# Kernel optimization log

Hardware: AMD Instinct MI355X
Metric: run time of the kernel (lower is better)

The kernel has to match this reference:

```python
import jax, jax.numpy as jnp
import numpy as np

NUM_SAMPLES = 128  # from __init__ default


def _trilinear_sample(vox, g):
    """grid_sample 5D, mode=bilinear (trilinear), padding_mode=zeros, align_corners=True.
    vox: [C, Dv, Hv, Wv]; g: [P, 3] normalized (x,y,z) with x->Wv, y->Hv, z->Dv.
    Returns [P, C]."""
    C, D, Hh, Ww = vox.shape
    x = (g[:, 0] + 1.0) * 0.5 * (Ww - 1)
    y = (g[:, 1] + 1.0) * 0.5 * (Hh - 1)
    z = (g[:, 2] + 1.0) * 0.5 * (D - 1)
    x0 = jnp.floor(x); y0 = jnp.floor(y); z0 = jnp.floor(z)
    xd = x - x0; yd = y - y0; zd = z - z0
    x0i = x0.astype(jnp.int32); y0i = y0.astype(jnp.int32); z0i = z0.astype(jnp.int32)
    out = jnp.zeros((g.shape[0], C), vox.dtype)
    for dz, wz in ((0, 1.0 - zd), (1, zd)):
        for dy, wy in ((0, 1.0 - yd), (1, yd)):
            for dx, wx in ((0, 1.0 - xd), (1, xd)):
                zi = z0i + dz; yi = y0i + dy; xi = x0i + dx
                valid = ((zi >= 0) & (zi < D) & (yi >= 0) & (yi < Hh) & (xi >= 0) & (xi < Ww)).astype(vox.dtype)
                zc = jnp.clip(zi, 0, D - 1); yc = jnp.clip(yi, 0, Hh - 1); xc = jnp.clip(xi, 0, Ww - 1)
                vals = vox[:, zc, yc, xc]  # [C, P]
                out = out + ((wz * wy * wx * valid)[:, None]) * vals.T
    return out


def setup_inputs() -> dict:
    key = jax.random.key(0)
    k1, k2 = jax.random.split(key)
    B, Hv, Wv, Dv = 4, 128, 128, 128
    H, W = 128, 128
    rgbsigma = jax.random.uniform(k1, (B, Hv, Wv, Dv, 4), dtype=jnp.float32)
    # cameras at ~z=3 looking down -z (identity rotation), slightly jittered
    pose = jnp.tile(jnp.eye(4, dtype=jnp.float32), (B, 1, 1))
    trans = jnp.array([0.0, 0.0, 3.0], dtype=jnp.float32) + 0.1 * jax.random.normal(k2, (B, 3), dtype=jnp.float32)
    pose = pose.at[:, :3, 3].set(trans)
    K = jnp.tile(jnp.array([[150.0, 0.0, 64.0], [0.0, 150.0, 64.0], [0.0, 0.0, 1.0]], dtype=jnp.float32), (B, 1, 1))
    bbox_min = jnp.tile(jnp.array([-1.0, -1.0, -1.0], dtype=jnp.float32), (B, 1))
    bbox_max = jnp.tile(jnp.array([1.0, 1.0, 1.0], dtype=jnp.float32), (B, 1))
    return {"rgbsigma": rgbsigma, "camera_pose": pose, "camera_intrinsics": K,
            "bbox_min": bbox_min, "bbox_max": bbox_max, "H": H, "W": W}


def reference(rgbsigma, camera_pose, camera_intrinsics, bbox_min, bbox_max, H, W):
    B = camera_pose.shape[0]
    N = H * W
    # --- ray generation ---
    ii, jj = jnp.meshgrid(jnp.arange(H, dtype=jnp.float32), jnp.arange(W, dtype=jnp.float32), indexing='ij')
    ii = ii.reshape(-1); jj = jj.reshape(-1)  # [N]
    fx = camera_intrinsics[:, 0, 0][:, None]; fy = camera_intrinsics[:, 1, 1][:, None]
    cx = camera_intrinsics[:, 0, 2][:, None]; cy = camera_intrinsics[:, 1, 2][:, None]
    dirs = jnp.stack([(jj[None, :] - cx) / fx, -(ii[None, :] - cy) / fy,
                      -jnp.ones((B, N), dtype=jnp.float32)], axis=-1)  # [B,N,3]
    rays_d = jnp.einsum('bij,bnj->bni', camera_pose[:, :3, :3], dirs)
    rays_d = rays_d / jnp.maximum(jnp.linalg.norm(rays_d, axis=-1, keepdims=True), 1e-12)
    rays_o = jnp.broadcast_to(camera_pose[:, None, :3, 3], (B, N, 3))
    # --- near/far via slab test ---
    inv_d = 1.0 / (rays_d + 1e-10)
    bmin = bbox_min[:, None, :]; bmax = bbox_max[:, None, :]
    t_min = (bmin - rays_o) * inv_d; t_max = (bmax - rays_o) * inv_d
    t1 = jnp.minimum(t_min, t_max); t2 = jnp.maximum(t_min, t_max)
    near = jnp.maximum(jnp.max(t1, axis=-1, keepdims=True), 0.1)
    far = jnp.maximum(jnp.min(t2, axis=-1, keepdims=True), near + 0.1)
    # --- stratified-uniform sample points ---
    t_vals = jnp.linspace(0.0, 1.0, NUM_SAMPLES, dtype=jnp.float32)
    z_vals = near + (far - near) * t_vals  # [B,N,M]
    pts = rays_o[:, :, None, :] + rays_d[:, :, None, :] * z_vals[..., None]  # [B,N,M,3]
    # --- trilinear voxel query ---
    scale = (bbox_max - bbox_min + 1e-10)[:, None, None, :]
    pts_norm = 2.0 * (pts - bbox_min[:, None, None, :]) / scale - 1.0
    vox = jnp.transpose(rgbsigma, (0, 4, 3, 1, 2))  # [B,4,Dv,Hv,Wv]
    sampled = jax.vmap(_trilinear_sample)(vox, pts_norm.reshape(B, N * NUM_SAMPLES, 3))
    sampled = sampled.reshape(B, N, NUM_SAMPLES, 4)
    rgb = sampled[..., :3]; sigma = sampled[..., 3]
    # --- alpha compositing ---
    dists = z_vals[..., 1:] - z_vals[..., :-1]
    dists = jnp.concatenate([dists, jnp.full_like(dists[..., :1], 1e10)], axis=-1)
    alpha = 1.0 - jnp.exp(-jax.nn.relu(sigma) * dists)
    trans = jnp.cumprod(jnp.concatenate([jnp.ones_like(alpha[..., :1]), 1.0 - alpha + 1e-10], axis=-1), axis=-1)[..., :-1]
    weights = alpha * trans
    rgb_map = jnp.sum(weights[..., None] * rgb, axis=-2)  # [B,N,3]
    acc_map = jnp.sum(weights, axis=-1)
    rgb_map = rgb_map + (1.0 - acc_map[..., None])  # white background
    return jnp.transpose(rgb_map.reshape(B, H, W, 3), (0, 3, 1, 2))
```

## Files before the change

### kernel.cpp

```cpp
#include <hip/hip_runtime.h>

#define NSAMP 128
#define VD 128

struct Corner8 {
    float4 v0, v1, v2, v3, v4, v5, v6, v7;
    float  w0, w1, w2, w3, w4, w5, w6, w7;
};

__device__ __forceinline__ void compute_ray_setup(
    int ray, int N, int W,
    const float* __restrict__ pose, const float* __restrict__ Kmat,
    const float* __restrict__ bmin, const float* __restrict__ bmax,
    float& axv, float& bxv, float& ayv, float& byv, float& azv, float& bzv,
    float& near, float& dt)
{
    const int b = ray / N;
    const int pix = ray - b * N;
    const int i = pix / W;
    const int j = pix - i * W;

    const float* P  = pose + b * 16;
    const float* Kb = Kmat + b * 9;
    const float fx = Kb[0], cx = Kb[2], fy = Kb[4], cy = Kb[5];

    const float dcx = ((float)j - cx) / fx;
    const float dcy = -((float)i - cy) / fy;
    const float dcz = -1.0f;

    float dx = P[0]*dcx + P[1]*dcy + P[2]*dcz;
    float dy = P[4]*dcx + P[5]*dcy + P[6]*dcz;
    float dz = P[8]*dcx + P[9]*dcy + P[10]*dcz;
    float nrm = sqrtf(dx*dx + dy*dy + dz*dz);
    nrm = fmaxf(nrm, 1e-12f);
    dx /= nrm; dy /= nrm; dz /= nrm;

    const float ox = P[3], oy = P[7], oz = P[11];

    const float bx0 = bmin[b*3+0], by0 = bmin[b*3+1], bz0 = bmin[b*3+2];
    const float bx1 = bmax[b*3+0], by1 = bmax[b*3+1], bz1 = bmax[b*3+2];

    const float ivx = 1.0f / (dx + 1e-10f);
    const float ivy = 1.0f / (dy + 1e-10f);
    const float ivz = 1.0f / (dz + 1e-10f);

    float ta, tb;
    ta = (bx0 - ox) * ivx; tb = (bx1 - ox) * ivx;
    const float t1x = fminf(ta, tb), t2x = fmaxf(ta, tb);
    ta = (by0 - oy) * ivy; tb = (by1 - oy) * ivy;
    const float t1y = fminf(ta, tb), t2y = fmaxf(ta, tb);
    ta = (bz0 - oz) * ivz; tb = (bz1 - oz) * ivz;
    const float t1z = fminf(ta, tb), t2z = fmaxf(ta, tb);

    near = fmaxf(fmaxf(t1x, fmaxf(t1y, t1z)), 0.1f);
    const float far = fmaxf(fminf(t2x, fminf(t2y, t2z)), near + 0.1f);

    const float sxs = (bx1 - bx0) + 1e-10f;
    const float sys = (by1 - by0) + 1e-10f;
    const float szs = (bz1 - bz0) + 1e-10f;
    const float C = (float)(VD - 1);
    axv = (ox - bx0) / sxs * C; bxv = dx / sxs * C;
    ayv = (oy - by0) / sys * C; byv = dy / sys * C;
    azv = (oz - bz0) / szs * C; bzv = dz / szs * C;

    dt = (far - near) * (1.0f / (float)(NSAMP - 1));
}

__global__ __launch_bounds__(256)
void RaySetup_kernel(const float* __restrict__ pose,
                     const float* __restrict__ Kmat,
                     const float* __restrict__ bmin,
                     const float* __restrict__ bmax,
                     const int* __restrict__ dH,
                     const int* __restrict__ dW,
                     float* __restrict__ rp,
                     int rays)
{
    const int ray = blockIdx.x * blockDim.x + threadIdx.x;
    if (ray >= rays) return;
    const int H = dH[0], W = dW[0];
    const int N = H * W;
    float axv, bxv, ayv, byv, azv, bzv, near, dt;
    compute_ray_setup(ray, N, W, pose, Kmat, bmin, bmax,
                      axv, bxv, ayv, byv, azv, bzv, near, dt);
    float4* o = reinterpret_cast<float4*>(rp + (size_t)ray * 8);
    o[0] = make_float4(axv, bxv, ayv, byv);
    o[1] = make_float4(azv, bzv, near, dt);
}

__device__ __forceinline__ void fetch_sample(
    Corner8& Bf, const float4* __restrict__ V4, float t,
    float axv, float bxv, float ayv, float byv, float azv, float bzv)
{
    const float xf = axv + bxv * t;
    const float yf = ayv + byv * t;
    const float zf = azv + bzv * t;
    const float x0f = floorf(xf), y0f = floorf(yf), z0f = floorf(zf);
    const float xd = xf - x0f, yd = yf - y0f, zd = zf - z0f;
    const int x0 = (int)x0f, y0 = (int)y0f, z0 = (int)z0f;
    const int x1 = x0 + 1, y1 = y0 + 1, z1 = z0 + 1;

    const int xc0 = min(max(x0, 0), VD - 1), xc1 = min(max(x1, 0), VD - 1);
    const int yc0 = min(max(y0, 0), VD - 1), yc1 = min(max(y1, 0), VD - 1);
    const int zc0 = min(max(z0, 0), VD - 1), zc1 = min(max(z1, 0), VD - 1);

    const float vx0 = (x0 == xc0) ? 1.0f : 0.0f;
    const float vx1 = (x1 == xc1) ? 1.0f : 0.0f;
    const float vy0 = (y0 == yc0) ? 1.0f : 0.0f;
    const float vy1 = (y1 == yc1) ? 1.0f : 0.0f;
    const float vz0 = (z0 == zc0) ? 1.0f : 0.0f;
    const float vz1 = (z1 == zc1) ? 1.0f : 0.0f;

    const float wx0 = (1.0f - xd) * vx0, wx1 = xd * vx1;
    const float wy0 = (1.0f - yd) * vy0, wy1 = yd * vy1;
    const float wz0 = (1.0f - zd) * vz0, wz1 = zd * vz1;

    const int r0 = yc0 << 14, r1 = yc1 << 14;
    const int c0 = xc0 << 7,  c1 = xc1 << 7;
    const int i00 = r0 + c0, i01 = r0 + c1;
    const int i10 = r1 + c0, i11 = r1 + c1;

    Bf.v0 = V4[i00 + zc0];
    Bf.v1 = V4[i00 + zc1];
    Bf.v2 = V4[i01 + zc0];
    Bf.v3 = V4[i01 + zc1];
    Bf.v4 = V4[i10 + zc0];
    Bf.v5 = V4[i10 + zc1];
    Bf.v6 = V4[i11 + zc0];
    Bf.v7 = V4[i11 + zc1];

    Bf.w0 = wy0 * wx0 * wz0;
    Bf.w1 = wy0 * wx0 * wz1;
    Bf.w2 = wy0 * wx1 * wz0;
    Bf.w3 = wy0 * wx1 * wz1;
    Bf.w4 = wy1 * wx0 * wz0;
    Bf.w5 = wy1 * wx0 * wz1;
    Bf.w6 = wy1 * wx1 * wz0;
    Bf.w7 = wy1 * wx1 * wz1;
}

__device__ __forceinline__ float4 interp_sample(const Corner8& Bf)
{
    float4 r;
    r.x = (Bf.w0*Bf.v0.x + Bf.w1*Bf.v1.x) + (Bf.w2*Bf.v2.x + Bf.w3*Bf.v3.x)
        + (Bf.w4*Bf.v4.x + Bf.w5*Bf.v5.x) + (Bf.w6*Bf.v6.x + Bf.w7*Bf.v7.x);
    r.y = (Bf.w0*Bf.v0.y + Bf.w1*Bf.v1.y) + (Bf.w2*Bf.v2.y + Bf.w3*Bf.v3.y)
        + (Bf.w4*Bf.v4.y + Bf.w5*Bf.v5.y) + (Bf.w6*Bf.v6.y + Bf.w7*Bf.v7.y);
    r.z = (Bf.w0*Bf.v0.z + Bf.w1*Bf.v1.z) + (Bf.w2*Bf.v2.z + Bf.w3*Bf.v3.z)
        + (Bf.w4*Bf.v4.z + Bf.w5*Bf.v5.z) + (Bf.w6*Bf.v6.z + Bf.w7*Bf.v7.z);
    r.w = (Bf.w0*Bf.v0.w + Bf.w1*Bf.v1.w) + (Bf.w2*Bf.v2.w + Bf.w3*Bf.v3.w)
        + (Bf.w4*Bf.v4.w + Bf.w5*Bf.v5.w) + (Bf.w6*Bf.v6.w + Bf.w7*Bf.v7.w);
    return r;
}

__device__ __forceinline__ void consume_set(
    const Corner8& C, int k, float dt, int sl,
    float& Tcarry, float& accR, float& accG, float& accB)
{
    const float4 s = interp_sample(C);
    const float sig = fmaxf(s.w, 0.0f);
    const float dist = (k == NSAMP - 1) ? 1e10f : dt;
    const float alpha = 1.0f - __expf(-sig * dist);
    float incl = 1.0f - alpha + 1e-10f;

    #pragma unroll
    for (int d = 1; d < 16; d <<= 1) {
        const float o = __shfl_up(incl, d, 16);
        if (sl >= d) incl *= o;
    }
    float P = __shfl_up(incl, 1, 16);
    if (sl == 0) P = 1.0f;

    const float w = alpha * P * Tcarry;
    accR += w * s.x;
    accG += w * s.y;
    accB += w * s.z;

    const float Ttot = __shfl(incl, 15, 16);
    Tcarry *= Ttot;
}

template <bool USE_WS>
__global__ __launch_bounds__(256, 1)
void VoxelRenderer_kernel(const float* __restrict__ vol,
                          const float* __restrict__ pose,
                          const float* __restrict__ Kmat,
                          const float* __restrict__ bmin,
                          const float* __restrict__ bmax,
                          const int* __restrict__ dH,
                          const int* __restrict__ dW,
                          const float* __restrict__ rayp,
                          float* __restrict__ out,
                          int rays)
{
    const int lane = threadIdx.x & 63;
    const int wq   = threadIdx.x >> 6;
    const int rq   = lane >> 4;
    const int sl   = lane & 15;

    const int nwg = gridDim.x;
    const int bid = blockIdx.x;
    const int q = nwg >> 3, r = nwg & 7;
    const int xcd = bid & 7, idx = bid >> 3;
    const int swz = (xcd < r ? xcd * (q + 1) : r * (q + 1) + (xcd - r) * q) + idx;

    const int H = dH[0], W = dW[0];
    const int N = H * W;
    const int quads = rays >> 2;
    const int qid = swz * 4 + wq;
    if (qid >= quads) return;

    const int qPerImg = N >> 2;
    const int b   = qid / qPerImg;
    const int rem = qid - b * qPerImg;
    const int halfW = W >> 1;
    const int qi = rem / halfW;
    const int qj = rem - qi * halfW;
    const int i = qi * 2 + (rq >> 1);
    const int j = qj * 2 + (rq & 1);
    const int ray = b * N + i * W + j;

    float axv, bxv, ayv, byv, azv, bzv, near, dt;
    if (USE_WS) {
        const float4* p = reinterpret_cast<const float4*>(rayp + (size_t)ray * 8);
        const float4 p0 = p[0];
        const float4 p1 = p[1];
        axv = p0.x; bxv = p0.y; ayv = p0.z; byv = p0.w;
        azv = p1.x; bzv = p1.y; near = p1.z; dt = p1.w;
    } else {
        compute_ray_setup(ray, N, W, pose, Kmat, bmin, bmax,
                          axv, bxv, ayv, byv, azv, bzv, near, dt);
    }

    const float4* __restrict__ V4 =
        reinterpret_cast<const float4*>(vol + (size_t)b * VD * VD * VD * 4);

    float Tcarry = 1.0f;
    float accR = 0.0f, accG = 0.0f, accB = 0.0f;

    Corner8 A, Bf;
    fetch_sample(A, V4, near + dt * (float)sl, axv, bxv, ayv, byv, azv, bzv);

    #pragma unroll
    for (int st = 0; st < 8; st += 2) {
        fetch_sample(Bf, V4, near + dt * (float)((st + 1) * 16 + sl),
                     axv, bxv, ayv, byv, azv, bzv);
        consume_set(A, st * 16 + sl, dt, sl, Tcarry, accR, accG, accB);
        if (st + 2 < 8)
            fetch_sample(A, V4, near + dt * (float)((st + 2) * 16 + sl),
                         axv, bxv, ayv, byv, azv, bzv);
        consume_set(Bf, (st + 1) * 16 + sl, dt, sl, Tcarry, accR, accG, accB);
    }

    #pragma unroll
    for (int d = 1; d < 16; d <<= 1) {
        accR += __shfl_xor(accR, d, 16);
        accG += __shfl_xor(accG, d, 16);
        accB += __shfl_xor(accB, d, 16);
    }

    if (sl == 0) {
        const float bg = Tcarry;
        float* outb = out + (size_t)b * 3 * N + i * W + j;
        outb[0 * (size_t)N] = accR + bg;
        outb[1 * (size_t)N] = accG + bg;
        outb[2 * (size_t)N] = accB + bg;
    }
}

extern "C" void kernel_launch(void* const* d_in, const int* in_sizes, int n_in,
                              void* d_out, int out_size, void* d_ws, size_t ws_size,
                              hipStream_t stream) {
    const float* rgbsigma = (const float*)d_in[0];
    const float* pose     = (const float*)d_in[1];
    const float* Kmat     = (const float*)d_in[2];
    const float* bmin     = (const float*)d_in[3];
    const float* bmax     = (const float*)d_in[4];
    const int*   dH       = (const int*)d_in[5];
    const int*   dW       = (const int*)d_in[6];
    float* out = (float*)d_out;

    const int rays  = out_size / 3;
    const int quads = rays / 4;
    const int grid  = (quads + 3) / 4;
    const bool use_ws = ws_size >= (size_t)rays * 8 * sizeof(float);

    if (use_ws) {
        float* rp = (float*)d_ws;
        RaySetup_kernel<<<(rays + 255) / 256, 256, 0, stream>>>(
            pose, Kmat, bmin, bmax, dH, dW, rp, rays);
        VoxelRenderer_kernel<true><<<grid, 256, 0, stream>>>(
            rgbsigma, pose, Kmat, bmin, bmax, dH, dW, rp, out, rays);
    } else {
        VoxelRenderer_kernel<false><<<grid, 256, 0, stream>>>(
            rgbsigma, pose, Kmat, bmin, bmax, dH, dW, nullptr, out, rays);
    }
}
```

Before: 56.40 us.

## Split ray compositing into two independent half-ray chains to deepen memory pipelining

Each ray's 128 samples are split into two independent halves, each with its own transmittance and color accumulators, so four sample sets are in flight instead of two. The halves are combined at the end using associative compositing (front color plus front transmittance times back color). This breaks the serial transmittance dependency and raises memory-level parallelism, at the cost of roughly doubling live registers for the corner buffers, which can reduce occupancy.

```diff
diff --git a/kernel.cpp b/kernel.cpp
--- a/kernel.cpp
+++ b/kernel.cpp
@@ -235,22 +235,35 @@
     const float4* __restrict__ V4 =
         reinterpret_cast<const float4*>(vol + (size_t)b * VD * VD * VD * 4);
 
-    float Tcarry = 1.0f;
-    float accR = 0.0f, accG = 0.0f, accB = 0.0f;
-
-    Corner8 A, Bf;
-    fetch_sample(A, V4, near + dt * (float)sl, axv, bxv, ayv, byv, azv, bzv);
-
-    #pragma unroll
-    for (int st = 0; st < 8; st += 2) {
-        fetch_sample(Bf, V4, near + dt * (float)((st + 1) * 16 + sl),
-                     axv, bxv, ayv, byv, azv, bzv);
-        consume_set(A, st * 16 + sl, dt, sl, Tcarry, accR, accG, accB);
-        if (st + 2 < 8)
-            fetch_sample(A, V4, near + dt * (float)((st + 2) * 16 + sl),
-                         axv, bxv, ayv, byv, azv, bzv);
-        consume_set(Bf, (st + 1) * 16 + sl, dt, sl, Tcarry, accR, accG, accB);
-    }
+    float T1 = 1.0f, T2 = 1.0f;
+    float r1R = 0.0f, r1G = 0.0f, r1B = 0.0f;
+    float r2R = 0.0f, r2G = 0.0f, r2B = 0.0f;
+
+    Corner8 A1, B1, A2, B2;
+    fetch_sample(A1, V4, near + dt * (float)(0 * 16 + sl), axv, bxv, ayv, byv, azv, bzv);
+    fetch_sample(A2, V4, near + dt * (float)(4 * 16 + sl), axv, bxv, ayv, byv, azv, bzv);
+    fetch_sample(B1, V4, near + dt * (float)(1 * 16 + sl), axv, bxv, ayv, byv, azv, bzv);
+    fetch_sample(B2, V4, near + dt * (float)(5 * 16 + sl), axv, bxv, ayv, byv, azv, bzv);
+
+    consume_set(A1, 0 * 16 + sl, dt, sl, T1, r1R, r1G, r1B);
+    consume_set(A2, 4 * 16 + sl, dt, sl, T2, r2R, r2G, r2B);
+    fetch_sample(A1, V4, near + dt * (float)(2 * 16 + sl), axv, bxv, ayv, byv, azv, bzv);
+    fetch_sample(A2, V4, near + dt * (float)(6 * 16 + sl), axv, bxv, ayv, byv, azv, bzv);
+
+    consume_set(B1, 1 * 16 + sl, dt, sl, T1, r1R, r1G, r1B);
+    consume_set(B2, 5 * 16 + sl, dt, sl, T2, r2R, r2G, r2B);
+    fetch_sample(B1, V4, near + dt * (float)(3 * 16 + sl), axv, bxv, ayv, byv, azv, bzv);
+    fetch_sample(B2, V4, near + dt * (float)(7 * 16 + sl), axv, bxv, ayv, byv, azv, bzv);
+
+    consume_set(A1, 2 * 16 + sl, dt, sl, T1, r1R, r1G, r1B);
+    consume_set(A2, 6 * 16 + sl, dt, sl, T2, r2R, r2G, r2B);
+
+    consume_set(B1, 3 * 16 + sl, dt, sl, T1, r1R, r1G, r1B);
+    consume_set(B2, 7 * 16 + sl, dt, sl, T2, r2R, r2G, r2B);
+
+    float accR = r1R + T1 * r2R;
+    float accG = r1G + T1 * r2G;
+    float accB = r1B + T1 * r2B;
 
     #pragma unroll
     for (int d = 1; d < 16; d <<= 1) {
@@ -260,7 +273,7 @@
     }
 
     if (sl == 0) {
-        const float bg = Tcarry;
+        const float bg = T1 * T2;
         float* outb = out + (size_t)b * 3 * N + i * W + j;
         outb[0 * (size_t)N] = accR + bg;
         outb[1 * (size_t)N] = accG + bg;
```

New measurement: 60.72 us. 1.08x slower.

## Map each wavefront to a 2x4 ray tile with 8 lanes per ray

Applied to the files above, without the earlier changes.

Each wavefront now handles 8 rays arranged in a 2x4 pixel tile, with 8 lanes per ray, where it previously handled 4 rays in a 2x2 quad with 16 lanes per ray. Each lane now processes 16 sample sets instead of 8, and the transmittance scan and final reductions run over width-8 groups. The aim is to double the work per wavefront, shorten the shuffle scans, and widen the footprint for voxel-cache locality. In exchange the grid is halved, which may reduce the latency hiding available for the gathers, and each lane runs a longer serial loop.

```diff
diff --git a/kernel.cpp b/kernel.cpp
--- a/kernel.cpp
+++ b/kernel.cpp
@@ -153,7 +153,7 @@
     return r;
 }
 
-__device__ __forceinline__ void consume_set(
+__device__ __forceinline__ void consume_set8(
     const Corner8& C, int k, float dt, int sl,
     float& Tcarry, float& accR, float& accG, float& accB)
 {
@@ -164,11 +164,11 @@
     float incl = 1.0f - alpha + 1e-10f;
 
     #pragma unroll
-    for (int d = 1; d < 16; d <<= 1) {
-        const float o = __shfl_up(incl, d, 16);
+    for (int d = 1; d < 8; d <<= 1) {
+        const float o = __shfl_up(incl, d, 8);
         if (sl >= d) incl *= o;
     }
-    float P = __shfl_up(incl, 1, 16);
+    float P = __shfl_up(incl, 1, 8);
     if (sl == 0) P = 1.0f;
 
     const float w = alpha * P * Tcarry;
@@ -176,8 +176,7 @@
     accG += w * s.y;
     accB += w * s.z;
 
-    const float Ttot = __shfl(incl, 15, 16);
-    Tcarry *= Ttot;
+    Tcarry *= __shfl(incl, 7, 8);
 }
 
 template <bool USE_WS>
@@ -195,8 +194,8 @@
 {
     const int lane = threadIdx.x & 63;
     const int wq   = threadIdx.x >> 6;
-    const int rq   = lane >> 4;
-    const int sl   = lane & 15;
+    const int rq   = lane >> 3;
+    const int sl   = lane & 7;
 
     const int nwg = gridDim.x;
     const int bid = blockIdx.x;
@@ -206,18 +205,18 @@
 
     const int H = dH[0], W = dW[0];
     const int N = H * W;
-    const int quads = rays >> 2;
-    const int qid = swz * 4 + wq;
-    if (qid >= quads) return;
-
-    const int qPerImg = N >> 2;
-    const int b   = qid / qPerImg;
-    const int rem = qid - b * qPerImg;
-    const int halfW = W >> 1;
-    const int qi = rem / halfW;
-    const int qj = rem - qi * halfW;
-    const int i = qi * 2 + (rq >> 1);
-    const int j = qj * 2 + (rq & 1);
+    const int tPerImg = (H >> 1) * (W >> 2);
+    const int tiles = (rays / N) * tPerImg;
+    const int tid = swz * 4 + wq;
+    if (tid >= tiles) return;
+
+    const int b   = tid / tPerImg;
+    const int rem = tid - b * tPerImg;
+    const int tCols = W >> 2;
+    const int ti = rem / tCols;
+    const int tj = rem - ti * tCols;
+    const int i = ti * 2 + (rq >> 2);
+    const int j = tj * 4 + (rq & 3);
     const int ray = b * N + i * W + j;
 
     float axv, bxv, ayv, byv, azv, bzv, near, dt;
@@ -242,21 +241,21 @@
     fetch_sample(A, V4, near + dt * (float)sl, axv, bxv, ayv, byv, azv, bzv);
 
     #pragma unroll
-    for (int st = 0; st < 8; st += 2) {
-        fetch_sample(Bf, V4, near + dt * (float)((st + 1) * 16 + sl),
+    for (int st = 0; st < 16; st += 2) {
+        fetch_sample(Bf, V4, near + dt * (float)((st + 1) * 8 + sl),
                      axv, bxv, ayv, byv, azv, bzv);
-        consume_set(A, st * 16 + sl, dt, sl, Tcarry, accR, accG, accB);
-        if (st + 2 < 8)
-            fetch_sample(A, V4, near + dt * (float)((st + 2) * 16 + sl),
+        consume_set8(A, st * 8 + sl, dt, sl, Tcarry, accR, accG, accB);
+        if (st + 2 < 16)
+            fetch_sample(A, V4, near + dt * (float)((st + 2) * 8 + sl),
                          axv, bxv, ayv, byv, azv, bzv);
-        consume_set(Bf, (st + 1) * 16 + sl, dt, sl, Tcarry, accR, accG, accB);
+        consume_set8(Bf, (st + 1) * 8 + sl, dt, sl, Tcarry, accR, accG, accB);
     }
 
     #pragma unroll
-    for (int d = 1; d < 16; d <<= 1) {
-        accR += __shfl_xor(accR, d, 16);
-        accG += __shfl_xor(accG, d, 16);
-        accB += __shfl_xor(accB, d, 16);
+    for (int d = 1; d < 8; d <<= 1) {
+        accR += __shfl_xor(accR, d, 8);
+        accG += __shfl_xor(accG, d, 8);
+        accB += __shfl_xor(accB, d, 8);
     }
 
     if (sl == 0) {
@@ -281,8 +280,8 @@
     float* out = (float*)d_out;
 
     const int rays  = out_size / 3;
-    const int quads = rays / 4;
-    const int grid  = (quads + 3) / 4;
+    const int tiles = rays / 8;
+    const int grid  = (tiles + 3) / 4;
     const bool use_ws = ws_size >= (size_t)rays * 8 * sizeof(float);
 
     if (use_ws) {
```

Result: slower. 68.62 us (+21.7%).
